# Performance work log

Measured on AMD Instinct MI355X. Metric: run time of the kernel, lower is better.

## Reference

```python
import jax, jax.numpy as jnp
import numpy as np

# ---- constants from init_kwargs ----
PC = (-51.2, -51.2, -5.0, 51.2, 51.2, 3.0)
D = 4          # num_points_in_pillar
ZMAX = 8       # Z default in gen_reference_points
BEV_H = 256; BEV_W = 256
Q = BEV_H * BEV_W
NUMCAM = 6
VBH = 256; VBW = 256
MAXLEN = VBH * VBW
MAX_OVER = 6
IMH, IMW = 512, 928   # data['img'].shape[2:]
EPS = 1e-5


def _gen_ref3d(bs):
    # gen_reference_points(dim='3d'): (bs, D, Q, 3), normalized coords
    zs = jnp.linspace(0.5, ZMAX - 0.5, D) / ZMAX
    xs = jnp.linspace(0.5, BEV_W - 0.5, BEV_W) / BEV_W
    ys = jnp.linspace(0.5, BEV_H - 0.5, BEV_H) / BEV_H
    g = jnp.stack([
        jnp.broadcast_to(xs[None, None, :], (D, BEV_H, BEV_W)),
        jnp.broadcast_to(ys[None, :, None], (D, BEV_H, BEV_W)),
        jnp.broadcast_to(zs[:, None, None], (D, BEV_H, BEV_W)),
    ], -1).reshape(D, Q, 3)
    return jnp.broadcast_to(g[None], (bs, D, Q, 3))


def setup_inputs() -> dict:
    key = jax.random.key(0)
    ego2img = jax.random.normal(key, (4, NUMCAM, 4, 4), dtype=jnp.float32)
    return {"ego2img": ego2img}


def reference(ego2img):
    B = ego2img.shape[0]
    ref = _gen_ref3d(B)                                   # (B,D,Q,3)
    x = ref[..., 0] * (PC[3] - PC[0]) + PC[0]
    y = ref[..., 1] * (PC[4] - PC[1]) + PC[1]
    z = ref[..., 2] * (PC[5] - PC[2]) + PC[2]
    pts = jnp.stack([x, y, z, jnp.ones_like(x)], -1)      # (B,D,Q,4) homogeneous

    # project each pillar point through each camera matrix
    cam = jnp.einsum('bcij,bdqj->bcdqi', ego2img, pts)    # (B,C,D,Q,4)
    zc = cam[..., 2]
    uv = cam[..., 0:2] / jnp.maximum(zc, EPS)[..., None]
    u = uv[..., 0] / IMW
    v = uv[..., 1] / IMH
    vis = (zc > EPS) & (v > 0.0) & (v < 1.0) & (u < 1.0) & (u > 0.0)  # (B,C,D,Q)
    rpc = jnp.clip(jnp.stack([u, v], -1), -2.1, 2.1)       # (B,C,D,Q,2)

    ref_cam = jnp.transpose(rpc, (1, 0, 3, 2, 4))          # (C,B,Q,D,2)
    vis_any = jnp.any(jnp.transpose(vis, (1, 0, 3, 2)), -1)  # (C,B,Q) pillar visible in cam

    qidx = jnp.arange(Q)
    qx = qidx % BEV_W
    qy = qidx // BEV_W
    # normalized BEV coords of each pillar (align_corners=True convention)
    gxy = jnp.stack([qx / (BEV_W - 1.0), qy / (BEV_H - 1.0)], -1) * 2.0 - 1.0

    # ---- queries_rebatch_grid: pack visible pillar coords densely per camera ----
    vis_bc = jnp.transpose(vis_any, (1, 0, 2)).reshape(B * NUMCAM, Q)

    def make_grid(vrow):
        rank = jnp.cumsum(vrow.astype(jnp.int32)) - 1      # position among visible pillars
        pos = jnp.where(vrow, rank, MAXLEN)                # invisible -> dummy slot
        buf = jnp.full((MAXLEN + 1, 2), -1.5, dtype=jnp.float32)
        return buf.at[pos].set(gxy)[:MAXLEN]

    grids = jax.vmap(make_grid)(vis_bc)                    # (B*C, MAXLEN, 2)
    queries_rebatch_grid = grids.reshape(B * NUMCAM, VBH, VBW, 2)

    # ---- reference_points_rebatch: grid_sample(nearest, align_corners=True, zeros pad) ----
    src = jnp.transpose(ref_cam.reshape(NUMCAM, B, Q, D * 2), (1, 0, 3, 2))
    src = src.reshape(B * NUMCAM, D * 2, Q)               # (B*C, D*2, H*W)
    ix = jnp.round((grids[..., 0] + 1.0) * 0.5 * (BEV_W - 1)).astype(jnp.int32)
    iy = jnp.round((grids[..., 1] + 1.0) * 0.5 * (BEV_H - 1)).astype(jnp.int32)
    ok = (ix >= 0) & (ix < BEV_W) & (iy >= 0) & (iy < BEV_H)
    gq = jnp.clip(iy * BEV_W + ix, 0, Q - 1)              # (B*C, MAXLEN)
    gathered = jnp.take_along_axis(src, gq[:, None, :], axis=2) * ok[:, None, :]
    reference_points_rebatch = jnp.transpose(gathered, (0, 2, 1)).reshape(
        B * NUMCAM, MAXLEN, D, 2)

    # ---- restore_bev_grid: map each (camera, pillar) slot back to dense BEV rows ----
    RB = MAX_OVER * BEV_H * BEV_W
    cam_off = jnp.arange(NUMCAM)[:, None] * VBH

    def make_restore(vis_b):  # (C, Q) bool
        vi = vis_b.astype(jnp.int32)
        rank = jnp.cumsum(vi, axis=1) - 1                  # packed index inside camera
        over = jnp.cumsum(vi, axis=0) - vi                 # overlap slot (exclusive count)
        gx = (rank % VBW) / (VBW - 1.0) * 2.0 - 1.0
        gy = (cam_off + rank // VBW) / (NUMCAM * VBH - 1.0) * 2.0 - 1.0
        flat = (over * BEV_H + qy[None]) * BEV_W + qx[None]
        flat = jnp.where(vis_b & (over < MAX_OVER), flat, RB)
        buf = jnp.full((RB + 1, 2), -1.5, dtype=jnp.float32)
        buf = buf.at[flat.reshape(-1)].set(jnp.stack([gx, gy], -1).reshape(-1, 2))
        return buf[:RB].reshape(MAX_OVER * BEV_H, BEV_W, 2)

    restore_bev_grid = jax.vmap(make_restore)(jnp.transpose(vis_any, (1, 0, 2)))

    # ---- bev_pillar_counts: 1 / (#cameras seeing each pillar) ----
    count = jnp.sum(vis_any.astype(jnp.float32), axis=0)   # (B, Q)
    bev_pillar_counts = (1.0 / jnp.maximum(count, 1.0))[..., None]

    return (queries_rebatch_grid, restore_bev_grid,
            reference_points_rebatch, bev_pillar_counts)
```

## Files before the change

kernel.cpp:

```cpp
#include <hip/hip_runtime.h>

#define NCAM      6
#define NB        4
#define NROWS     24
#define NQ        65536
#define MAXLEN_   65536

#define OFF_QGRID   0
#define OFF_RESTORE 3145728
#define OFF_REFPTS  6291456
#define OFF_COUNTS  18874368

__device__ __forceinline__ float zval(int d) {
    const float z[4] = { -4.5f, -2.16666674613952637f,
                          0.166666507720947266f, 2.5f };
    return z[d];
}

__device__ __forceinline__ float clip21(float x) {
    return fminf(fmaxf(x, -2.1f), 2.1f);
}

__device__ __forceinline__ bool proj_point(const float m[12], float x, float y, float z,
                                           float& u, float& v) {
    float c0 = ((m[0]*x + m[1]*y) + m[2]*z) + m[3];
    float c1 = ((m[4]*x + m[5]*y) + m[6]*z) + m[7];
    float c2 = ((m[8]*x + m[9]*y) + m[10]*z) + m[11];
    float zcl = fmaxf(c2, 1e-5f);
    float inv = __builtin_amdgcn_rcpf(zcl);
    u = (c0 * inv) * (1.0f / 928.0f);
    v = (c1 * inv) * (1.0f / 512.0f);
    return (c2 > 1e-5f) & (c1 > 0.0f) & (c1 < 512.0f * zcl)
         & (c0 > 0.0f) & (c0 < 928.0f * zcl);
}

__device__ __forceinline__ void load_mat(const float* __restrict__ ego2img, int row, float m[12]) {
    const float* M = ego2img + row * 16;
    #pragma unroll
    for (int i = 0; i < 12; ++i) m[i] = M[i];
}

__device__ __forceinline__ void bev_xy(int qx, int qy, float& x, float& y) {
    x = ((float)qx + 0.5f) * (1.0f/256.0f) * 102.4f - 51.2f;
    y = ((float)qy + 0.5f) * (1.0f/256.0f) * 102.4f - 51.2f;
}

__global__ void __launch_bounds__(256)
k_count(const float* __restrict__ ego2img, int* __restrict__ chunkCounts)
{
    int chunk = blockIdx.x, row = blockIdx.y;
    float m[12]; load_mat(ego2img, row, m);
    int t = threadIdx.x;
    int lane = t & 63;
    int q0 = chunk * 1024 + t * 4;
    int cnt = 0;
    #pragma unroll
    for (int i = 0; i < 4; ++i) {
        int q = q0 + i;
        float x, y; bev_xy(q & 255, q >> 8, x, y);
        bool va = false;
        #pragma unroll
        for (int d = 0; d < 4; ++d) {
            float u, v;
            va |= proj_point(m, x, y, zval(d), u, v);
        }
        unsigned long long bal = __ballot(va);
        if (lane == 0) cnt += __popcll(bal);
    }
    if (lane == 0)
        chunkCounts[row * 256 + chunk * 4 + (t >> 6)] = cnt;
}

__global__ void __launch_bounds__(256)
k_fused(const float* __restrict__ ego2img, const int* __restrict__ chunkCounts,
        float* __restrict__ out)
{
    int chunk = blockIdx.x, b = blockIdx.y;
    int t = threadIdx.x;
    int lane = t & 63, wid = t >> 6;
    unsigned long long lt = (1ull << lane) - 1ull;

    __shared__ int sBase[NCAM], sTotal[NCAM];
    __shared__ int waveCnt[NCAM][4];
    __shared__ float2 srow[NCAM][256];

    for (int c = wid; c < NCAM; c += 4) {
        const int* p = chunkCounts + (b * NCAM + c) * 256;
        int4 v4 = ((const int4*)p)[lane];
        int s = v4.x + v4.y + v4.z + v4.w;
        int incl = s;
        #pragma unroll
        for (int off = 1; off < 64; off <<= 1) {
            int n = __shfl_up(incl, off, 64);
            if (lane >= off) incl += n;
        }
        if (lane == (chunk >> 2)) {
            int base = incl - s;
            int k = chunk & 3;
            if (k > 0) base += v4.x;
            if (k > 1) base += v4.y;
            if (k > 2) base += v4.z;
            sBase[c] = base;
        }
        if (lane == 63) sTotal[c] = incl;
    }

    int q  = chunk * 256 + t;
    int qx = t, qy = chunk;
    float x, y; bev_xy(qx, qy, x, y);

    int rnk[NCAM];

    #pragma unroll
    for (int c = 0; c < NCAM; ++c) {
        float m[12]; load_mat(ego2img, b * NCAM + c, m);
        float uv[8];
        bool vis = false;
        #pragma unroll
        for (int d = 0; d < 4; ++d) {
            float u, v;
            bool vi = proj_point(m, x, y, zval(d), u, v);
            uv[2*d]   = clip21(u);
            uv[2*d+1] = clip21(v);
            vis |= vi;
        }
        unsigned long long bal = __ballot(vis);
        if (lane == 0) waveCnt[c][wid] = __popcll(bal);
        __syncthreads();

        int wbase = 0;
        #pragma unroll
        for (int w = 0; w < 3; ++w) if (w < wid) wbase += waveCnt[c][w];
        int r = sBase[c] + wbase + __popcll(bal & lt);

        float2* qgrid  = (float2*)(out + OFF_QGRID)  + (size_t)(b * NCAM + c) * MAXLEN_;
        float4* refpF4 = (float4*)(out + OFF_REFPTS) + (size_t)(b * NCAM + c) * (MAXLEN_ * 2);

        if (vis) {
            float2 g;
            g.x = ((float)qx / 255.0f) * 2.0f - 1.0f;
            g.y = ((float)qy / 255.0f) * 2.0f - 1.0f;
            qgrid[r] = g;
            refpF4[2*r]     = make_float4(uv[0], uv[1], uv[2], uv[3]);
            refpF4[2*r + 1] = make_float4(uv[4], uv[5], uv[6], uv[7]);
            rnk[c] = r;
        } else {
            rnk[c] = -1;
        }

        int s0 = max(sTotal[c], chunk << 8);
        int n  = ((chunk + 1) << 8) - s0;
        if (n > 0) {
            for (int i = t; i < n; i += 256)
                qgrid[s0 + i] = make_float2(-1.5f, -1.5f);
            float4 z4 = make_float4(0.f, 0.f, 0.f, 0.f);
            for (int i = t; i < 2 * n; i += 256)
                refpF4[2*s0 + i] = z4;
        }
    }

    int over = 0;
    #pragma unroll
    for (int c = 0; c < NCAM; ++c) {
        int r = rnk[c];
        if (r >= 0) {
            float gx = ((float)(r & 255) / 255.0f) * 2.0f - 1.0f;
            float gy = ((float)(c * 256 + (r >> 8)) / 1535.0f) * 2.0f - 1.0f;
            srow[over][t] = make_float2(gx, gy);
            ++over;
        }
    }
    for (int o = over; o < NCAM; ++o)
        srow[o][t] = make_float2(-1.5f, -1.5f);
    out[OFF_COUNTS + b * NQ + q] = 1.0f / fmaxf((float)over, 1.0f);
    __syncthreads();

    float2* rest = (float2*)(out + OFF_RESTORE) + (size_t)b * NCAM * NQ;
    #pragma unroll
    for (int o = 0; o < NCAM; ++o)
        rest[(o * 256 + qy) * 256 + t] = srow[o][t];
}

extern "C" void kernel_launch(void* const* d_in, const int* in_sizes, int n_in,
                              void* d_out, int out_size, void* d_ws, size_t ws_size,
                              hipStream_t stream)
{
    const float* ego2img = (const float*)d_in[0];
    float* out = (float*)d_out;
    int* chunkCounts = (int*)d_ws;

    k_count<<<dim3(64, NROWS), 256, 0, stream>>>(ego2img, chunkCounts);
    k_fused<<<dim3(256, NB),   256, 0, stream>>>(ego2img, chunkCounts, out);
}
```

Before: 90.43 us.

## Assign one wave per camera in fused kernel, removing per-camera block barriers

The fused kernel now launches 384 threads, so each of the six waves handles one camera and walks the 256 pillars of the BEV row in four 64-wide steps. Packed ranks come from a running wave-level ballot instead of shared wave counts, which removes the six per-camera __syncthreads and the serial camera loop. Each wave also does its own prefix scan and tail fill. Restore-grid slot selection and pillar counts are rebuilt from a shared rank table after one barrier, which adds redundant shared-memory reads across waves.

New measurement: 90.48 us. About the same (+0.1%).

```diff
diff --git a/kernel.cpp b/kernel.cpp
--- a/kernel.cpp
+++ b/kernel.cpp
@@ -71,49 +71,47 @@
         chunkCounts[row * 256 + chunk * 4 + (t >> 6)] = cnt;
 }
 
-__global__ void __launch_bounds__(256)
+__global__ void __launch_bounds__(384)
 k_fused(const float* __restrict__ ego2img, const int* __restrict__ chunkCounts,
         float* __restrict__ out)
 {
     int chunk = blockIdx.x, b = blockIdx.y;
     int t = threadIdx.x;
-    int lane = t & 63, wid = t >> 6;
+    int lane = t & 63;
+    int c = t >> 6;
     unsigned long long lt = (1ull << lane) - 1ull;
 
-    __shared__ int sBase[NCAM], sTotal[NCAM];
-    __shared__ int waveCnt[NCAM][4];
-    __shared__ float2 srow[NCAM][256];
+    __shared__ int lrank[NCAM][256];
 
-    for (int c = wid; c < NCAM; c += 4) {
-        const int* p = chunkCounts + (b * NCAM + c) * 256;
-        int4 v4 = ((const int4*)p)[lane];
-        int s = v4.x + v4.y + v4.z + v4.w;
-        int incl = s;
-        #pragma unroll
-        for (int off = 1; off < 64; off <<= 1) {
-            int n = __shfl_up(incl, off, 64);
-            if (lane >= off) incl += n;
-        }
-        if (lane == (chunk >> 2)) {
-            int base = incl - s;
-            int k = chunk & 3;
-            if (k > 0) base += v4.x;
-            if (k > 1) base += v4.y;
-            if (k > 2) base += v4.z;
-            sBase[c] = base;
-        }
-        if (lane == 63) sTotal[c] = incl;
+    int row = __builtin_amdgcn_readfirstlane(b * NCAM + c);
+
+    const int* p = chunkCounts + row * 256;
+    int4 v4 = ((const int4*)p)[lane];
+    int s = v4.x + v4.y + v4.z + v4.w;
+    int incl = s;
+    #pragma unroll
+    for (int off = 1; off < 64; off <<= 1) {
+        int nn = __shfl_up(incl, off, 64);
+        if (lane >= off) incl += nn;
     }
+    int k = chunk & 3;
+    int bb = incl - s + ((k > 0) ? v4.x : 0)
+                      + ((k > 1) ? v4.y : 0)
+                      + ((k > 2) ? v4.z : 0);
+    int base  = __shfl(bb,   chunk >> 2, 64);
+    int total = __shfl(incl, 63,        64);
 
-    int q  = chunk * 256 + t;
-    int qx = t, qy = chunk;
-    float x, y; bev_xy(qx, qy, x, y);
+    float m[12]; load_mat(ego2img, row, m);
 
-    int rnk[NCAM];
+    float2* qgrid  = (float2*)(out + OFF_QGRID)  + (size_t)row * MAXLEN_;
+    float4* refpF4 = (float4*)(out + OFF_REFPTS) + (size_t)row * (MAXLEN_ * 2);
+
+    int qy = chunk;
 
     #pragma unroll
-    for (int c = 0; c < NCAM; ++c) {
-        float m[12]; load_mat(ego2img, b * NCAM + c, m);
+    for (int i = 0; i < 4; ++i) {
+        int qx = i * 64 + lane;
+        float x, y; bev_xy(qx, qy, x, y);
         float uv[8];
         bool vis = false;
         #pragma unroll
@@ -125,17 +123,7 @@
             vis |= vi;
         }
         unsigned long long bal = __ballot(vis);
-        if (lane == 0) waveCnt[c][wid] = __popcll(bal);
-        __syncthreads();
-
-        int wbase = 0;
-        #pragma unroll
-        for (int w = 0; w < 3; ++w) if (w < wid) wbase += waveCnt[c][w];
-        int r = sBase[c] + wbase + __popcll(bal & lt);
-
-        float2* qgrid  = (float2*)(out + OFF_QGRID)  + (size_t)(b * NCAM + c) * MAXLEN_;
-        float4* refpF4 = (float4*)(out + OFF_REFPTS) + (size_t)(b * NCAM + c) * (MAXLEN_ * 2);
-
+        int r = base + __popcll(bal & lt);
         if (vis) {
             float2 g;
             g.x = ((float)qx / 255.0f) * 2.0f - 1.0f;
@@ -143,42 +131,45 @@
             qgrid[r] = g;
             refpF4[2*r]     = make_float4(uv[0], uv[1], uv[2], uv[3]);
             refpF4[2*r + 1] = make_float4(uv[4], uv[5], uv[6], uv[7]);
-            rnk[c] = r;
-        } else {
-            rnk[c] = -1;
         }
-
-        int s0 = max(sTotal[c], chunk << 8);
-        int n  = ((chunk + 1) << 8) - s0;
-        if (n > 0) {
-            for (int i = t; i < n; i += 256)
-                qgrid[s0 + i] = make_float2(-1.5f, -1.5f);
-            float4 z4 = make_float4(0.f, 0.f, 0.f, 0.f);
-            for (int i = t; i < 2 * n; i += 256)
-                refpF4[2*s0 + i] = z4;
-        }
+        lrank[c][qx] = vis ? r : -1;
+        base += __popcll(bal);
     }
 
-    int over = 0;
-    #pragma unroll
-    for (int c = 0; c < NCAM; ++c) {
-        int r = rnk[c];
-        if (r >= 0) {
-            float gx = ((float)(r & 255) / 255.0f) * 2.0f - 1.0f;
-            float gy = ((float)(c * 256 + (r >> 8)) / 1535.0f) * 2.0f - 1.0f;
-            srow[over][t] = make_float2(gx, gy);
-            ++over;
-        }
+    int s0 = max(total, chunk << 8);
+    int n  = ((chunk + 1) << 8) - s0;
+    if (n > 0) {
+        for (int j = lane; j < n; j += 64)
+            qgrid[s0 + j] = make_float2(-1.5f, -1.5f);
+        float4 z4 = make_float4(0.f, 0.f, 0.f, 0.f);
+        for (int j = lane; j < 2 * n; j += 64)
+            refpF4[2*s0 + j] = z4;
     }
-    for (int o = over; o < NCAM; ++o)
-        srow[o][t] = make_float2(-1.5f, -1.5f);
-    out[OFF_COUNTS + b * NQ + q] = 1.0f / fmaxf((float)over, 1.0f);
+
     __syncthreads();
 
     float2* rest = (float2*)(out + OFF_RESTORE) + (size_t)b * NCAM * NQ;
+    int o = c;
     #pragma unroll
-    for (int o = 0; o < NCAM; ++o)
-        rest[(o * 256 + qy) * 256 + t] = srow[o][t];
+    for (int i = 0; i < 4; ++i) {
+        int qx = i * 64 + lane;
+        float2 val = make_float2(-1.5f, -1.5f);
+        int cnt = 0;
+        #pragma unroll
+        for (int cc = 0; cc < NCAM; ++cc) {
+            int r = lrank[cc][qx];
+            bool v = (r >= 0);
+            if (v && (cnt == o)) {
+                val.x = ((float)(r & 255) / 255.0f) * 2.0f - 1.0f;
+                val.y = ((float)(cc * 256 + (r >> 8)) / 1535.0f) * 2.0f - 1.0f;
+            }
+            cnt += v;
+        }
+        rest[(o * 256 + qy) * 256 + qx] = val;
+        if (c == 0)
+            out[OFF_COUNTS + (size_t)b * NQ + qy * 256 + qx] =
+                1.0f / fmaxf((float)cnt, 1.0f);
+    }
 }
 
 extern "C" void kernel_launch(void* const* d_in, const int* in_sizes, int n_in,
@@ -190,5 +181,5 @@
     int* chunkCounts = (int*)d_ws;
 
     k_count<<<dim3(64, NROWS), 256, 0, stream>>>(ego2img, chunkCounts);
-    k_fused<<<dim3(256, NB),   256, 0, stream>>>(ego2img, chunkCounts, out);
+    k_fused<<<dim3(256, NB),   384, 0, stream>>>(ego2img, chunkCounts, out);
 }
```
